# Kernel tuning notes

Hardware: AMD Instinct MI355X
Metric: run time of the kernel (lower is better)

Reference implementation:

```python
import jax, jax.numpy as jnp
import numpy as np
from jax import lax

EPS = 1e-08


def setup_inputs() -> dict:
    key = jax.random.key(0)
    k1, k2, k3, k4 = jax.random.split(key, 4)
    b, cin, cout, hw, kk = 32, 256, 256, 64, 3
    fan_in = cin * kk * kk
    # kaiming_normal_(a=0, mode='fan_in', nonlinearity='leaky_relu') -> gain=sqrt(2), std=sqrt(2/fan_in)
    w_std = np.sqrt(2.0 / fan_in).astype(np.float32)
    return {
        "x": jax.random.normal(k1, (b, cin, hw, hw), dtype=jnp.float32),
        "y": jax.random.normal(k2, (b, cin), dtype=jnp.float32),
        "weight": jax.random.normal(k3, (cout, cin, kk, kk), dtype=jnp.float32) * w_std,
        "bias": jax.random.normal(k4, (cout,), dtype=jnp.float32) * 0.1,
    }


def _modulated_conv(x, y, weight, bias):
    # x: [b, cin, h, w]; y: [b, cin]; weight: [cout, cin, kh, kw]; bias: [cout]
    # modulate: per-sample scale of input channels
    w = weight[None] * (y[:, None, :, None, None] + 1.0)  # [b, cout, cin, kh, kw]
    # demodulate: normalize each (sample, out-channel) filter
    d = lax.rsqrt(jnp.sum(w * w, axis=(2, 3, 4), keepdims=True) + EPS)
    w = w * d

    def conv_one(xi, wi):
        # xi: [cin, h, w]; wi: [cout, cin, kh, kw]
        out = lax.conv_general_dilated(
            xi[None], wi, window_strides=(1, 1), padding="SAME",
            dimension_numbers=("NCHW", "OIHW", "NCHW"))
        return out[0]  # [cout, h, w]

    out = jax.vmap(conv_one)(x, w)  # [b, cout, h, w]
    return out + bias[None, :, None, None]


def reference(x, y, weight, bias):
    return _modulated_conv(x, y, weight, bias)
```

## Files before the change

kernel.cpp:

```cpp
#include <hip/hip_runtime.h>
#include <hip/hip_bf16.h>

typedef __attribute__((ext_vector_type(8))) short short8;
typedef __attribute__((ext_vector_type(4))) float f32x4;

#define XT_IMG_BYTES (66*66*256*2)
#define XT_TOTAL_BYTES (32LL*XT_IMG_BYTES)
#define WM_ROW_BYTES (2304*2)
#define WM_IMG_BYTES (256*WM_ROW_BYTES)

static __device__ __forceinline__ void async16(void* lds, const void* g) {
  __builtin_amdgcn_global_load_lds((const __attribute__((address_space(1))) void*)g,
                                   (__attribute__((address_space(3))) void*)lds, 16, 0, 0);
}
static __device__ __forceinline__ ushort f2bf(float f) {
  __hip_bfloat16 h = __float2bfloat16(f);
  return *reinterpret_cast<ushort*>(&h);
}

__global__ __launch_bounds__(256) void k_zeroborder(uint4* __restrict__ xT4) {
  const int b = blockIdx.x >> 3;
  const int t = ((blockIdx.x & 7) << 8) | threadIdx.x;
  const uint4 z = make_uint4(0u, 0u, 0u, 0u);
  uint4* base = xT4 + (size_t)b * (66 * 66 * 32);
  uint4* r0  = base;
  uint4* r65 = base + (size_t)65 * 66 * 32;
  for (int i = t; i < 2112; i += 2048) { r0[i] = z; r65[i] = z; }
  {
    int r = (t >> 5) + 1, c = t & 31;
    base[((size_t)r * 66 + 0)  * 32 + c] = z;
    base[((size_t)r * 66 + 65) * 32 + c] = z;
  }
}

__global__ __launch_bounds__(256) void k_xpose(const float* __restrict__ x,
                                               ushort* __restrict__ xT) {
  __shared__ float lds[64][65];
  const int bx = blockIdx.x;
  const int b  = bx >> 8;
  const int h  = (bx >> 2) & 63;
  const int c0 = (bx & 3) << 6;
  const int t  = threadIdx.x;
  const int tw = t & 63, tg = t >> 6;
  const float* xp = x + (size_t)(b * 256 + c0) * 4096 + h * 64 + tw;
#pragma unroll
  for (int j = 0; j < 16; ++j) {
    int il = j * 4 + tg;
    lds[il][tw] = xp[(size_t)il * 4096];
  }
  __syncthreads();
  const int q  = t & 7;
  const int w0 = t >> 3;
  ushort* op = xT + (size_t)b * (66 * 66 * 256) + ((size_t)(h + 1) * 66 + 1) * 256 + c0;
#pragma unroll
  for (int j = 0; j < 2; ++j) {
    const int wl = j * 32 + w0;
    short8 v;
#pragma unroll
    for (int k2 = 0; k2 < 8; ++k2) v[k2] = (short)f2bf(lds[8 * q + k2][wl]);
    *(short8*)(op + (size_t)wl * 256 + 8 * q) = v;
  }
}

__global__ __launch_bounds__(256) void k_modw(const float* __restrict__ W,
                                              const float* __restrict__ y,
                                              ushort* __restrict__ wmod) {
  __shared__ float red[256];
  const int b = blockIdx.x >> 8, o = blockIdx.x & 255, t = threadIdx.x;
  const float* wp = W + (size_t)(o * 256 + t) * 9;
  float wr[9];
#pragma unroll
  for (int r = 0; r < 9; ++r) wr[r] = wp[r];
  const float ym = y[b * 256 + t] + 1.0f;
  float ss = 0.f;
#pragma unroll
  for (int r = 0; r < 9; ++r) ss += wr[r] * wr[r];
  red[t] = ss * ym * ym;
  __syncthreads();
  for (int s = 128; s > 0; s >>= 1) {
    if (t < s) red[t] += red[t + s];
    __syncthreads();
  }
  const float sc = rsqrtf(red[0] + 1e-8f) * ym;
  ushort* op = wmod + (size_t)(b * 256 + o) * 2304 + t;
#pragma unroll
  for (int r = 0; r < 9; ++r) op[r * 256] = f2bf(wr[r] * sc);
}

__global__ __launch_bounds__(512, 2) void k_gemm(const ushort* __restrict__ wmod,
                                                 const ushort* __restrict__ xT,
                                                 const float* __restrict__ bias,
                                                 float* __restrict__ out) {
  __shared__ ushort ldsA[2][16384];
  __shared__ ushort ldsB[2][16384];

  const int t  = threadIdx.x;
  const int bx = blockIdx.x;
  const int xcd = bx & 7;
  const int idx = bx >> 3;
  const int b   = xcd + ((idx >> 4) << 3);
  const int tn  = idx & 15;
  const int n0  = tn << 8;
  const int h0  = tn << 2;

  const int ln = t & 15;
  const int kq = (t >> 4) & 3;
  const int wv = t >> 6;
  const int wm = wv >> 2;
  const int wn = wv & 3;

  const char* wmodB = (const char*)wmod + (size_t)b * WM_IMG_BYTES;
  const char* xTB   = (const char*)xT   + (size_t)b * XT_IMG_BYTES;

  int gAoff[4], gBoff[4];
#pragma unroll
  for (int j = 0; j < 4; ++j) {
    const int s = j * 512 + t;
    const int row = s >> 3, g = s & 7;
    gAoff[j] = row * WM_ROW_BYTES + ((g ^ (row & 7)) << 4);
    const int hr = row >> 6, wc = row & 63;
    gBoff[j] = ((h0 + hr) * 66 + wc) * 512 + ((g ^ (row & 7)) << 4);
  }

  const int swz = ln & 7;
  const int g0 = ((0 | kq) ^ swz) << 3;
  const int g1 = ((4 | kq) ^ swz) << 3;
  const int aBase = (wm * 128 + ln) * 64;
  const int bBase = (wn * 64  + ln) * 64;

  f32x4 acc[8][4];
  const f32x4 z4 = {0.f, 0.f, 0.f, 0.f};
#pragma unroll
  for (int i = 0; i < 8; ++i)
#pragma unroll
    for (int j = 0; j < 4; ++j) acc[i][j] = z4;

#define STAGE(KT, BUF) do {                                              \
    const int r_  = (KT) >> 2;                                           \
    const int c2_ = ((KT) & 3) << 7;            \
    const int kh_ = r_ / 3;                                              \
    const int kw_ = r_ - kh_ * 3;                                        \
    const int koA_ = r_ * 512 + c2_;                                     \
    const int koB_ = (kh_ * 66 + kw_) * 512 + c2_;                       \
    ushort* la_ = &ldsA[BUF][0];                                         \
    ushort* lb_ = &ldsB[BUF][0];                                         \
    async16(la_ + (0 * 512 + t) * 8, wmodB + gAoff[0] + koA_);           \
    async16(lb_ + (0 * 512 + t) * 8, xTB   + gBoff[0] + koB_);           \
    async16(la_ + (1 * 512 + t) * 8, wmodB + gAoff[1] + koA_);           \
    async16(lb_ + (1 * 512 + t) * 8, xTB   + gBoff[1] + koB_);           \
    async16(la_ + (2 * 512 + t) * 8, wmodB + gAoff[2] + koA_);           \
    async16(lb_ + (2 * 512 + t) * 8, xTB   + gBoff[2] + koB_);           \
    async16(la_ + (3 * 512 + t) * 8, wmodB + gAoff[3] + koA_);           \
    async16(lb_ + (3 * 512 + t) * 8, xTB   + gBoff[3] + koB_);           \
  } while (0)

#define MF(F, E, A, B) acc[F][E] = __builtin_amdgcn_mfma_f32_16x16x32_bf16(A, B, acc[F][E], 0, 0, 0)

#define KHALF(GOFF) do {                                                 \
    const ushort* qa = bufA + aBase + (GOFF);                            \
    const ushort* qb = bufB + bBase + (GOFF);                            \
    short8 b0 = *(const short8*)(qb);                                    \
    short8 b1 = *(const short8*)(qb + 1024);                             \
    short8 b2 = *(const short8*)(qb + 2048);                             \
    short8 b3 = *(const short8*)(qb + 3072);                             \
    short8 a0 = *(const short8*)(qa);                                    \
    short8 a1 = *(const short8*)(qa + 1024);                             \
    short8 a2 = *(const short8*)(qa + 2048);                             \
    short8 a3 = *(const short8*)(qa + 3072);                             \
    short8 a4 = *(const short8*)(qa + 4096);                             \
    short8 a5 = *(const short8*)(qa + 5120);                             \
    short8 a6 = *(const short8*)(qa + 6144);                             \
    short8 a7 = *(const short8*)(qa + 7168);                             \
    __builtin_amdgcn_s_setprio(1);                                       \
    MF(0,0,a0,b0); MF(1,0,a1,b0); MF(2,0,a2,b0); MF(3,0,a3,b0);          \
    MF(4,0,a4,b0); MF(5,0,a5,b0); MF(6,0,a6,b0); MF(7,0,a7,b0);          \
    MF(0,1,a0,b1); MF(1,1,a1,b1); MF(2,1,a2,b1); MF(3,1,a3,b1);          \
    MF(4,1,a4,b1); MF(5,1,a5,b1); MF(6,1,a6,b1); MF(7,1,a7,b1);          \
    MF(0,2,a0,b2); MF(1,2,a1,b2); MF(2,2,a2,b2); MF(3,2,a3,b2);          \
    MF(4,2,a4,b2); MF(5,2,a5,b2); MF(6,2,a6,b2); MF(7,2,a7,b2);          \
    MF(0,3,a0,b3); MF(1,3,a1,b3); MF(2,3,a2,b3); MF(3,3,a3,b3);          \
    MF(4,3,a4,b3); MF(5,3,a5,b3); MF(6,3,a6,b3); MF(7,3,a7,b3);          \
    __builtin_amdgcn_s_setprio(0);                                       \
  } while (0)

  STAGE(0, 0);
  int cur = 0;
#pragma unroll 1
  for (int kt = 0; kt < 36; ++kt) {
    if (kt < 35) {
      STAGE(kt + 1, cur ^ 1);
      asm volatile("s_waitcnt vmcnt(8)" ::: "memory");
    } else {
      asm volatile("s_waitcnt vmcnt(0)" ::: "memory");
    }
    __builtin_amdgcn_s_barrier();
    __builtin_amdgcn_sched_barrier(0);
    {
      const ushort* bufA = &ldsA[cur][0];
      const ushort* bufB = &ldsB[cur][0];
      KHALF(g0);
      KHALF(g1);
    }
    __builtin_amdgcn_sched_barrier(0);
    __builtin_amdgcn_s_barrier();
    cur ^= 1;
  }

  const float* bp = bias + wm * 128;
  float* outB = out + ((size_t)(b * 256 + wm * 128)) * 4096 + n0 + wn * 64 + ln;
#pragma unroll
  for (int mi = 0; mi < 8; ++mi) {
#pragma unroll
    for (int rg = 0; rg < 4; ++rg) {
      const int orow = mi * 16 + kq * 4 + rg;
      const float bv = bp[orow];
      float* po = outB + (size_t)orow * 4096;
#pragma unroll
      for (int ni = 0; ni < 4; ++ni) po[ni * 16] = acc[mi][ni][rg] + bv;
    }
  }
#undef STAGE
#undef MF
#undef KHALF
}

extern "C" void kernel_launch(void* const* d_in, const int* in_sizes, int n_in,
                              void* d_out, int out_size, void* d_ws, size_t ws_size,
                              hipStream_t stream) {
  const float* x    = (const float*)d_in[0];
  const float* y    = (const float*)d_in[1];
  const float* W    = (const float*)d_in[2];
  const float* bias = (const float*)d_in[3];
  float* out = (float*)d_out;

  ushort* xT   = (ushort*)d_ws;
  ushort* wmod = (ushort*)((char*)d_ws + (size_t)XT_TOTAL_BYTES);

  k_zeroborder<<<256,         256, 0, stream>>>((uint4*)d_ws);
  k_xpose     <<<32 * 64 * 4, 256, 0, stream>>>(x, xT);
  k_modw      <<<32 * 256,    256, 0, stream>>>(W, y, wmod);
  k_gemm      <<<512,         512, 0, stream>>>(wmod, xT, bias, out);
}
```

Baseline: 395.2 us.

## Fuse prep kernels into one launch and interleave GEMM loads with MFMA phases

The border-zeroing, transpose and weight-modulation kernels are merged into a single launch that branches on block index, which removes two kernel launches. The GEMM main loop is split into four phases. Each phase loads LDS fragments, issues part of the next tile's global-to-LDS copies (A first, then B), and then runs 16 MFMAs between barriers, with one full vmcnt wait per iteration. This spreads memory traffic across the compute phases but adds four times as many barriers per k-step.

```diff
diff --git a/kernel.cpp b/kernel.cpp
--- a/kernel.cpp
+++ b/kernel.cpp
@@ -18,73 +18,76 @@
   return *reinterpret_cast<ushort*>(&h);
 }
 
-__global__ __launch_bounds__(256) void k_zeroborder(uint4* __restrict__ xT4) {
-  const int b = blockIdx.x >> 3;
-  const int t = ((blockIdx.x & 7) << 8) | threadIdx.x;
-  const uint4 z = make_uint4(0u, 0u, 0u, 0u);
-  uint4* base = xT4 + (size_t)b * (66 * 66 * 32);
-  uint4* r0  = base;
-  uint4* r65 = base + (size_t)65 * 66 * 32;
-  for (int i = t; i < 2112; i += 2048) { r0[i] = z; r65[i] = z; }
-  {
-    int r = (t >> 5) + 1, c = t & 31;
-    base[((size_t)r * 66 + 0)  * 32 + c] = z;
-    base[((size_t)r * 66 + 65) * 32 + c] = z;
-  }
-}
-
-__global__ __launch_bounds__(256) void k_xpose(const float* __restrict__ x,
-                                               ushort* __restrict__ xT) {
-  __shared__ float lds[64][65];
-  const int bx = blockIdx.x;
-  const int b  = bx >> 8;
-  const int h  = (bx >> 2) & 63;
-  const int c0 = (bx & 3) << 6;
-  const int t  = threadIdx.x;
-  const int tw = t & 63, tg = t >> 6;
-  const float* xp = x + (size_t)(b * 256 + c0) * 4096 + h * 64 + tw;
-#pragma unroll
-  for (int j = 0; j < 16; ++j) {
-    int il = j * 4 + tg;
-    lds[il][tw] = xp[(size_t)il * 4096];
-  }
-  __syncthreads();
-  const int q  = t & 7;
-  const int w0 = t >> 3;
-  ushort* op = xT + (size_t)b * (66 * 66 * 256) + ((size_t)(h + 1) * 66 + 1) * 256 + c0;
-#pragma unroll
-  for (int j = 0; j < 2; ++j) {
-    const int wl = j * 32 + w0;
-    short8 v;
-#pragma unroll
-    for (int k2 = 0; k2 < 8; ++k2) v[k2] = (short)f2bf(lds[8 * q + k2][wl]);
-    *(short8*)(op + (size_t)wl * 256 + 8 * q) = v;
-  }
-}
-
-__global__ __launch_bounds__(256) void k_modw(const float* __restrict__ W,
+__global__ __launch_bounds__(256) void k_prep(const float* __restrict__ x,
+                                              const float* __restrict__ W,
                                               const float* __restrict__ y,
+                                              ushort* __restrict__ xT,
                                               ushort* __restrict__ wmod) {
-  __shared__ float red[256];
-  const int b = blockIdx.x >> 8, o = blockIdx.x & 255, t = threadIdx.x;
-  const float* wp = W + (size_t)(o * 256 + t) * 9;
-  float wr[9];
-#pragma unroll
-  for (int r = 0; r < 9; ++r) wr[r] = wp[r];
-  const float ym = y[b * 256 + t] + 1.0f;
-  float ss = 0.f;
-#pragma unroll
-  for (int r = 0; r < 9; ++r) ss += wr[r] * wr[r];
-  red[t] = ss * ym * ym;
-  __syncthreads();
-  for (int s = 128; s > 0; s >>= 1) {
-    if (t < s) red[t] += red[t + s];
+  __shared__ float smem[64][65];
+  const int bid = blockIdx.x;
+  const int t   = threadIdx.x;
+
+  if (bid < 8192) {
+    const int b  = bid >> 8;
+    const int h  = (bid >> 2) & 63;
+    const int c0 = (bid & 3) << 6;
+    const int tw = t & 63, tg = t >> 6;
+    const float* xp = x + (size_t)(b * 256 + c0) * 4096 + h * 64 + tw;
+#pragma unroll
+    for (int j = 0; j < 16; ++j) {
+      int il = j * 4 + tg;
+      smem[il][tw] = xp[(size_t)il * 4096];
+    }
     __syncthreads();
-  }
-  const float sc = rsqrtf(red[0] + 1e-8f) * ym;
-  ushort* op = wmod + (size_t)(b * 256 + o) * 2304 + t;
-#pragma unroll
-  for (int r = 0; r < 9; ++r) op[r * 256] = f2bf(wr[r] * sc);
+    const int q  = t & 7;
+    const int w0 = t >> 3;
+    ushort* op = xT + (size_t)b * (66 * 66 * 256) + ((size_t)(h + 1) * 66 + 1) * 256 + c0;
+#pragma unroll
+    for (int j = 0; j < 2; ++j) {
+      const int wl = j * 32 + w0;
+      short8 v;
+#pragma unroll
+      for (int k2 = 0; k2 < 8; ++k2) v[k2] = (short)f2bf(smem[8 * q + k2][wl]);
+      *(short8*)(op + (size_t)wl * 256 + 8 * q) = v;
+    }
+  } else if (bid < 16384) {
+    float* red = &smem[0][0];
+    const int bb = bid - 8192;
+    const int b = bb >> 8, o = bb & 255;
+    const float* wp = W + (size_t)(o * 256 + t) * 9;
+    float wr[9];
+#pragma unroll
+    for (int r = 0; r < 9; ++r) wr[r] = wp[r];
+    const float ym = y[b * 256 + t] + 1.0f;
+    float ss = 0.f;
+#pragma unroll
+    for (int r = 0; r < 9; ++r) ss += wr[r] * wr[r];
+    red[t] = ss * ym * ym;
+    __syncthreads();
+    for (int s = 128; s > 0; s >>= 1) {
+      if (t < s) red[t] += red[t + s];
+      __syncthreads();
+    }
+    const float sc = rsqrtf(red[0] + 1e-8f) * ym;
+    ushort* op = wmod + (size_t)(b * 256 + o) * 2304 + t;
+#pragma unroll
+    for (int r = 0; r < 9; ++r) op[r * 256] = f2bf(wr[r] * sc);
+  } else {
+    const int zb = bid - 16384;
+    const int b  = zb >> 3;
+    const int tt = ((zb & 7) << 8) | t;
+    uint4* xT4 = (uint4*)xT;
+    const uint4 z = make_uint4(0u, 0u, 0u, 0u);
+    uint4* base = xT4 + (size_t)b * (66 * 66 * 32);
+    uint4* r0  = base;
+    uint4* r65 = base + (size_t)65 * 66 * 32;
+    for (int i = tt; i < 2112; i += 2048) { r0[i] = z; r65[i] = z; }
+    {
+      int r = (tt >> 5) + 1, c = tt & 31;
+      base[((size_t)r * 66 + 0)  * 32 + c] = z;
+      base[((size_t)r * 66 + 65) * 32 + c] = z;
+    }
+  }
 }
 
 __global__ __launch_bounds__(512, 2) void k_gemm(const ushort* __restrict__ wmod,
@@ -135,75 +138,108 @@
 #pragma unroll
     for (int j = 0; j < 4; ++j) acc[i][j] = z4;
 
-#define STAGE(KT, BUF) do {                                              \
-    const int r_  = (KT) >> 2;                                           \
-    const int c2_ = ((KT) & 3) << 7;            \
-    const int kh_ = r_ / 3;                                              \
-    const int kw_ = r_ - kh_ * 3;                                        \
-    const int koA_ = r_ * 512 + c2_;                                     \
-    const int koB_ = (kh_ * 66 + kw_) * 512 + c2_;                       \
-    ushort* la_ = &ldsA[BUF][0];                                         \
-    ushort* lb_ = &ldsB[BUF][0];                                         \
-    async16(la_ + (0 * 512 + t) * 8, wmodB + gAoff[0] + koA_);           \
-    async16(lb_ + (0 * 512 + t) * 8, xTB   + gBoff[0] + koB_);           \
-    async16(la_ + (1 * 512 + t) * 8, wmodB + gAoff[1] + koA_);           \
-    async16(lb_ + (1 * 512 + t) * 8, xTB   + gBoff[1] + koB_);           \
-    async16(la_ + (2 * 512 + t) * 8, wmodB + gAoff[2] + koA_);           \
-    async16(lb_ + (2 * 512 + t) * 8, xTB   + gBoff[2] + koB_);           \
-    async16(la_ + (3 * 512 + t) * 8, wmodB + gAoff[3] + koA_);           \
-    async16(lb_ + (3 * 512 + t) * 8, xTB   + gBoff[3] + koB_);           \
+#define STAGE_A(KO, BUF) do {                                        \
+    ushort* la_ = &ldsA[BUF][0];                                     \
+    async16(la_ + (0 * 512 + t) * 8, wmodB + gAoff[0] + (KO));       \
+    async16(la_ + (1 * 512 + t) * 8, wmodB + gAoff[1] + (KO));       \
+    async16(la_ + (2 * 512 + t) * 8, wmodB + gAoff[2] + (KO));       \
+    async16(la_ + (3 * 512 + t) * 8, wmodB + gAoff[3] + (KO));       \
   } while (0)
+#define STAGE_B(KO, BUF) do {                                        \
+    ushort* lb_ = &ldsB[BUF][0];                                     \
+    async16(lb_ + (0 * 512 + t) * 8, xTB + gBoff[0] + (KO));         \
+    async16(lb_ + (1 * 512 + t) * 8, xTB + gBoff[1] + (KO));         \
+    async16(lb_ + (2 * 512 + t) * 8, xTB + gBoff[2] + (KO));         \
+    async16(lb_ + (3 * 512 + t) * 8, xTB + gBoff[3] + (KO));         \
+  } while (0)
 
 #define MF(F, E, A, B) acc[F][E] = __builtin_amdgcn_mfma_f32_16x16x32_bf16(A, B, acc[F][E], 0, 0, 0)
-
-#define KHALF(GOFF) do {                                                 \
-    const ushort* qa = bufA + aBase + (GOFF);                            \
-    const ushort* qb = bufB + bBase + (GOFF);                            \
-    short8 b0 = *(const short8*)(qb);                                    \
-    short8 b1 = *(const short8*)(qb + 1024);                             \
-    short8 b2 = *(const short8*)(qb + 2048);                             \
-    short8 b3 = *(const short8*)(qb + 3072);                             \
-    short8 a0 = *(const short8*)(qa);                                    \
-    short8 a1 = *(const short8*)(qa + 1024);                             \
-    short8 a2 = *(const short8*)(qa + 2048);                             \
-    short8 a3 = *(const short8*)(qa + 3072);                             \
-    short8 a4 = *(const short8*)(qa + 4096);                             \
-    short8 a5 = *(const short8*)(qa + 5120);                             \
-    short8 a6 = *(const short8*)(qa + 6144);                             \
-    short8 a7 = *(const short8*)(qa + 7168);                             \
-    __builtin_amdgcn_s_setprio(1);                                       \
-    MF(0,0,a0,b0); MF(1,0,a1,b0); MF(2,0,a2,b0); MF(3,0,a3,b0);          \
-    MF(4,0,a4,b0); MF(5,0,a5,b0); MF(6,0,a6,b0); MF(7,0,a7,b0);          \
-    MF(0,1,a0,b1); MF(1,1,a1,b1); MF(2,1,a2,b1); MF(3,1,a3,b1);          \
-    MF(4,1,a4,b1); MF(5,1,a5,b1); MF(6,1,a6,b1); MF(7,1,a7,b1);          \
-    MF(0,2,a0,b2); MF(1,2,a1,b2); MF(2,2,a2,b2); MF(3,2,a3,b2);          \
-    MF(4,2,a4,b2); MF(5,2,a5,b2); MF(6,2,a6,b2); MF(7,2,a7,b2);          \
-    MF(0,3,a0,b3); MF(1,3,a1,b3); MF(2,3,a2,b3); MF(3,3,a3,b3);          \
-    MF(4,3,a4,b3); MF(5,3,a5,b3); MF(6,3,a6,b3); MF(7,3,a7,b3);          \
-    __builtin_amdgcn_s_setprio(0);                                       \
-  } while (0)
-
-  STAGE(0, 0);
+#define FENCE() __builtin_amdgcn_sched_barrier(0)
+#define BAR()   __builtin_amdgcn_s_barrier()
+
+  STAGE_A(0, 0);
+  STAGE_B(0, 0);
+  asm volatile("s_waitcnt vmcnt(0)" ::: "memory");
+  BAR();
+
   int cur = 0;
 #pragma unroll 1
   for (int kt = 0; kt < 36; ++kt) {
-    if (kt < 35) {
-      STAGE(kt + 1, cur ^ 1);
-      asm volatile("s_waitcnt vmcnt(8)" ::: "memory");
-    } else {
-      asm volatile("s_waitcnt vmcnt(0)" ::: "memory");
-    }
-    __builtin_amdgcn_s_barrier();
-    __builtin_amdgcn_sched_barrier(0);
-    {
-      const ushort* bufA = &ldsA[cur][0];
-      const ushort* bufB = &ldsB[cur][0];
-      KHALF(g0);
-      KHALF(g1);
-    }
-    __builtin_amdgcn_sched_barrier(0);
-    __builtin_amdgcn_s_barrier();
-    cur ^= 1;
+    const int nk  = kt + 1;
+    const int r_  = nk >> 2;
+    const int c2_ = (nk & 3) << 7;
+    const int kh_ = r_ / 3;
+    const int kw_ = r_ - kh_ * 3;
+    const int koA = r_ * 512 + c2_;
+    const int koB = (kh_ * 66 + kw_) * 512 + c2_;
+    const ushort* bufA = &ldsA[cur][0];
+    const ushort* bufB = &ldsB[cur][0];
+    const int nb = cur ^ 1;
+
+    short8 A0 = *(const short8*)(bufA + aBase + 0 * 1024 + g0);
+    short8 A1 = *(const short8*)(bufA + aBase + 1 * 1024 + g0);
+    short8 A2 = *(const short8*)(bufA + aBase + 2 * 1024 + g0);
+    short8 A3 = *(const short8*)(bufA + aBase + 3 * 1024 + g0);
+    short8 B0 = *(const short8*)(bufB + bBase + 0 * 1024 + g0);
+    short8 B1 = *(const short8*)(bufB + bBase + 1 * 1024 + g0);
+    short8 B2 = *(const short8*)(bufB + bBase + 2 * 1024 + g0);
+    short8 B3 = *(const short8*)(bufB + bBase + 3 * 1024 + g0);
+    if (kt < 35) STAGE_A(koA, nb);
+    FENCE(); BAR(); FENCE();
+    __builtin_amdgcn_s_setprio(1);
+    MF(0,0,A0,B0); MF(1,0,A1,B0); MF(2,0,A2,B0); MF(3,0,A3,B0);
+    MF(0,1,A0,B1); MF(1,1,A1,B1); MF(2,1,A2,B1); MF(3,1,A3,B1);
+    MF(0,2,A0,B2); MF(1,2,A1,B2); MF(2,2,A2,B2); MF(3,2,A3,B2);
+    MF(0,3,A0,B3); MF(1,3,A1,B3); MF(2,3,A2,B3); MF(3,3,A3,B3);
+    __builtin_amdgcn_s_setprio(0);
+    FENCE(); BAR();
+
+    short8 A4 = *(const short8*)(bufA + aBase + 4 * 1024 + g0);
+    short8 A5 = *(const short8*)(bufA + aBase + 5 * 1024 + g0);
+    short8 A6 = *(const short8*)(bufA + aBase + 6 * 1024 + g0);
+    short8 A7 = *(const short8*)(bufA + aBase + 7 * 1024 + g0);
+    if (kt < 35) STAGE_B(koB, nb);
+    FENCE(); BAR(); FENCE();
+    __builtin_amdgcn_s_setprio(1);
+    MF(4,0,A4,B0); MF(5,0,A5,B0); MF(6,0,A6,B0); MF(7,0,A7,B0);
+    MF(4,1,A4,B1); MF(5,1,A5,B1); MF(6,1,A6,B1); MF(7,1,A7,B1);
+    MF(4,2,A4,B2); MF(5,2,A5,B2); MF(6,2,A6,B2); MF(7,2,A7,B2);
+    MF(4,3,A4,B3); MF(5,3,A5,B3); MF(6,3,A6,B3); MF(7,3,A7,B3);
+    __builtin_amdgcn_s_setprio(0);
+    FENCE(); BAR();
+
+    short8 C0 = *(const short8*)(bufA + aBase + 0 * 1024 + g1);
+    short8 C1 = *(const short8*)(bufA + aBase + 1 * 1024 + g1);
+    short8 C2 = *(const short8*)(bufA + aBase + 2 * 1024 + g1);
+    short8 C3 = *(const short8*)(bufA + aBase + 3 * 1024 + g1);
+    short8 D0 = *(const short8*)(bufB + bBase + 0 * 1024 + g1);
+    short8 D1 = *(const short8*)(bufB + bBase + 1 * 1024 + g1);
+    short8 D2 = *(const short8*)(bufB + bBase + 2 * 1024 + g1);
+    short8 D3 = *(const short8*)(bufB + bBase + 3 * 1024 + g1);
+    FENCE(); BAR(); FENCE();
+    __builtin_amdgcn_s_setprio(1);
+    MF(0,0,C0,D0); MF(1,0,C1,D0); MF(2,0,C2,D0); MF(3,0,C3,D0);
+    MF(0,1,C0,D1); MF(1,1,C1,D1); MF(2,1,C2,D1); MF(3,1,C3,D1);
+    MF(0,2,C0,D2); MF(1,2,C1,D2); MF(2,2,C2,D2); MF(3,2,C3,D2);
+    MF(0,3,C0,D3); MF(1,3,C1,D3); MF(2,3,C2,D3); MF(3,3,C3,D3);
+    __builtin_amdgcn_s_setprio(0);
+    FENCE(); BAR();
+
+    short8 C4 = *(const short8*)(bufA + aBase + 4 * 1024 + g1);
+    short8 C5 = *(const short8*)(bufA + aBase + 5 * 1024 + g1);
+    short8 C6 = *(const short8*)(bufA + aBase + 6 * 1024 + g1);
+    short8 C7 = *(const short8*)(bufA + aBase + 7 * 1024 + g1);
+    asm volatile("s_waitcnt vmcnt(0)" ::: "memory");
+    FENCE(); BAR(); FENCE();
+    __builtin_amdgcn_s_setprio(1);
+    MF(4,0,C4,D0); MF(5,0,C5,D0); MF(6,0,C6,D0); MF(7,0,C7,D0);
+    MF(4,1,C4,D1); MF(5,1,C5,D1); MF(6,1,C6,D1); MF(7,1,C7,D1);
+    MF(4,2,C4,D2); MF(5,2,C5,D2); MF(6,2,C6,D2); MF(7,2,C7,D2);
+    MF(4,3,C4,D3); MF(5,3,C5,D3); MF(6,3,C6,D3); MF(7,3,C7,D3);
+    __builtin_amdgcn_s_setprio(0);
+    FENCE(); BAR();
+
+    cur = nb;
   }
 
   const float* bp = bias + wm * 128;
@@ -219,9 +255,11 @@
       for (int ni = 0; ni < 4; ++ni) po[ni * 16] = acc[mi][ni][rg] + bv;
     }
   }
-#undef STAGE
+#undef STAGE_A
+#undef STAGE_B
 #undef MF
-#undef KHALF
+#undef FENCE
+#undef BAR
 }
 
 extern "C" void kernel_launch(void* const* d_in, const int* in_sizes, int n_in,
@@ -236,8 +274,6 @@
   ushort* xT   = (ushort*)d_ws;
   ushort* wmod = (ushort*)((char*)d_ws + (size_t)XT_TOTAL_BYTES);
 
-  k_zeroborder<<<256,         256, 0, stream>>>((uint4*)d_ws);
-  k_xpose     <<<32 * 64 * 4, 256, 0, stream>>>(x, xT);
-  k_modw      <<<32 * 256,    256, 0, stream>>>(W, y, wmod);
-  k_gemm      <<<512,         512, 0, stream>>>(wmod, xT, bias, out);
-}
+  k_prep<<<16640, 256, 0, stream>>>(x, W, y, xT, wmod);
+  k_gemm<<<512,   512, 0, stream>>>(wmod, xT, bias, out);
+}
```

Result: faster. 374.9 us (-5.1%).
